# Kernel tuning notes

Measured on AMD Instinct MI355X. Metric: run time of the kernel, lower is better.

Reference implementation:

```python
import jax, jax.numpy as jnp
import numpy as np

N_NODES = 50000
N_EDGES = 800000
IN_CH = 128
OUT_CH = 64
HID = 2 * OUT_CH  # 128
NEG_SLOPE = 0.2  # PyG GATConv default negative_slope


def gat_conv(x, edge_index, W, a_src, a_dst, b):
    """Single-head PyG GATConv (heads=1, concat=True, self-loops already in edge_index)."""
    N = x.shape[0]
    h = x @ W  # [N, C]
    src, dst = edge_index[0], edge_index[1]
    # per-edge attention logits: leaky_relu(a_src . h_src + a_dst . h_dst)
    e = jax.nn.leaky_relu((h @ a_src)[src] + (h @ a_dst)[dst], NEG_SLOPE)  # [E]
    # softmax over incoming edges of each dst node (numerically stable)
    m = jax.ops.segment_max(e, dst, num_segments=N)
    p = jnp.exp(e - m[dst])
    denom = jax.ops.segment_sum(p, dst, num_segments=N)
    coef = p / denom[dst]  # [E]
    # scatter-aggregate weighted source features
    out = jax.ops.segment_sum(coef[:, None] * h[src], dst, num_segments=N)  # [N, C]
    return out + b


def setup_inputs() -> dict:
    key = jax.random.key(0)
    ks = jax.random.split(key, 12)
    s_in = 1.0 / np.sqrt(IN_CH)
    s_h = 1.0 / np.sqrt(HID)
    return {
        "x": jax.random.normal(ks[0], (N_NODES, IN_CH), dtype=jnp.float32),
        "edge_index": jax.random.randint(ks[1], (2, N_EDGES), 0, N_NODES, dtype=jnp.int64),
        "W1": jax.random.normal(ks[2], (IN_CH, HID), dtype=jnp.float32) * s_in,
        "a_src1": jax.random.normal(ks[3], (HID,), dtype=jnp.float32) * s_h,
        "a_dst1": jax.random.normal(ks[4], (HID,), dtype=jnp.float32) * s_h,
        "b1": jnp.zeros((HID,), dtype=jnp.float32),
        "W_mu": jax.random.normal(ks[5], (HID, OUT_CH), dtype=jnp.float32) * s_h,
        "a_src_mu": jax.random.normal(ks[6], (OUT_CH,), dtype=jnp.float32) * 0.125,
        "a_dst_mu": jax.random.normal(ks[7], (OUT_CH,), dtype=jnp.float32) * 0.125,
        "b_mu": jnp.zeros((OUT_CH,), dtype=jnp.float32),
        "W_ls": jax.random.normal(ks[8], (HID, OUT_CH), dtype=jnp.float32) * s_h,
        "a_src_ls": jax.random.normal(ks[9], (OUT_CH,), dtype=jnp.float32) * 0.125,
        "a_dst_ls": jax.random.normal(ks[10], (OUT_CH,), dtype=jnp.float32) * 0.125,
        "b_ls": jnp.zeros((OUT_CH,), dtype=jnp.float32),
    }


def reference(x, edge_index, W1, a_src1, a_dst1, b1, W_mu, a_src_mu, a_dst_mu, b_mu, W_ls, a_src_ls, a_dst_ls, b_ls):
    N = x.shape[0]
    loops = jnp.arange(N, dtype=edge_index.dtype)
    ei = jnp.concatenate([edge_index, jnp.stack([loops, loops])], axis=1)  # add self-loops
    h = jax.nn.relu(gat_conv(x, ei, W1, a_src1, a_dst1, b1))
    mu = gat_conv(h, ei, W_mu, a_src_mu, a_dst_mu, b_mu)
    logstd = gat_conv(h, ei, W_ls, a_src_ls, a_dst_ls, b_ls)
    return mu, logstd
```

## Files before the change

kernel.cpp:

```cpp
#include <hip/hip_runtime.h>
#include <hip/hip_bf16.h>
#include <math.h>

typedef __attribute__((ext_vector_type(8))) _Float16 half8;
typedef __attribute__((ext_vector_type(4))) float f32x4;


__device__ __forceinline__ float wave_max64(float v) {
#pragma unroll
  for (int o = 32; o > 0; o >>= 1) v = fmaxf(v, __shfl_xor(v, o));
  return v;
}
__device__ __forceinline__ float wave_sum64(float v) {
#pragma unroll
  for (int o = 32; o > 0; o >>= 1) v += __shfl_xor(v, o);
  return v;
}
__device__ __forceinline__ float leaky02(float v) { return v > 0.0f ? v : 0.2f * v; }

__device__ __forceinline__ unsigned short f2bf(float f) {
  unsigned u = __float_as_uint(f);
  u += 0x7FFF + ((u >> 16) & 1);
  return (unsigned short)(u >> 16);
}
__device__ __forceinline__ float2 bfp(unsigned v) {
  float2 r;
  r.x = __uint_as_float(v << 16);
  r.y = __uint_as_float(v & 0xFFFF0000u);
  return r;
}


#define BSHIFT 9
#define BDSTS 512

__global__ __launch_bounds__(256) void bucket_hist_kernel(
    const int* __restrict__ ei, int* __restrict__ bcount, int E, int NBUCK) {
  __shared__ int h[128];
  if (threadIdx.x < 128) h[threadIdx.x] = 0;
  __syncthreads();
  for (int e = blockIdx.x * blockDim.x + threadIdx.x; e < E; e += gridDim.x * blockDim.x)
    atomicAdd(&h[ei[E + e] >> BSHIFT], 1);
  __syncthreads();
  if (threadIdx.x < NBUCK && h[threadIdx.x]) atomicAdd(&bcount[threadIdx.x], h[threadIdx.x]);
}

__global__ __launch_bounds__(128) void bucket_scan_kernel(
    const int* __restrict__ bcount, int* __restrict__ bstart, int* __restrict__ bcursor,
    int* __restrict__ row_start, int NBUCK, int E, int N) {
  __shared__ int lds[128];
  int t = threadIdx.x;
  int v = (t < NBUCK) ? bcount[t] : 0;
  lds[t] = v;
  __syncthreads();
#pragma unroll
  for (int off = 1; off < 128; off <<= 1) {
    int tmp = (t >= off) ? lds[t - off] : 0;
    __syncthreads();
    lds[t] += tmp;
    __syncthreads();
  }
  if (t < NBUCK) {
    int excl = lds[t] - v;
    bstart[t] = excl;
    bcursor[t] = excl;
  }
  if (t == 0) { bstart[NBUCK] = E; row_start[N] = E; }
}

#define CHUNK 4096
__global__ __launch_bounds__(256) void pair_scatter_kernel(
    const int* __restrict__ ei, int* __restrict__ bcursor, int2* __restrict__ pairs, int E) {
  __shared__ int h[128], base[128], cur[128];
  if (threadIdx.x < 128) { h[threadIdx.x] = 0; cur[threadIdx.x] = 0; }
  __syncthreads();
  int c0 = blockIdx.x * CHUNK;
  int c1 = min(c0 + CHUNK, E);
  for (int e = c0 + (int)threadIdx.x; e < c1; e += 256)
    atomicAdd(&h[ei[E + e] >> BSHIFT], 1);
  __syncthreads();
  if (threadIdx.x < 128 && h[threadIdx.x])
    base[threadIdx.x] = atomicAdd(&bcursor[threadIdx.x], h[threadIdx.x]);
  __syncthreads();
  for (int e = c0 + (int)threadIdx.x; e < c1; e += 256) {
    int dst = ei[E + e];
    int src = ei[e];
    int b = dst >> BSHIFT;
    int r = atomicAdd(&cur[b], 1);
    pairs[base[b] + r] = make_int2(src, dst);
  }
}

__global__ __launch_bounds__(512) void fine_kernel(
    const int2* __restrict__ pairs, const int* __restrict__ bstart,
    int* __restrict__ row_start, int* __restrict__ esrc, int N) {
  __shared__ int h[BDSTS], sc[BDSTS], cur[BDSTS];
  int t = threadIdx.x;
  int b = blockIdx.x;
  int d0 = b << BSHIFT;
  int d1 = min(d0 + BDSTS, N);
  int beg = bstart[b], end = bstart[b + 1];
  h[t] = 0;
  __syncthreads();
  for (int i = beg + t; i < end; i += 512) atomicAdd(&h[pairs[i].y - d0], 1);
  __syncthreads();
  int v = h[t];
  sc[t] = v;
  __syncthreads();
#pragma unroll
  for (int off = 1; off < BDSTS; off <<= 1) {
    int tmp = (t >= off) ? sc[t - off] : 0;
    __syncthreads();
    sc[t] += tmp;
    __syncthreads();
  }
  int excl = sc[t] - v;
  if (d0 + t < d1) row_start[d0 + t] = beg + excl;
  cur[t] = excl;
  __syncthreads();
  for (int i = beg + t; i < end; i += 512) {
    int2 p = pairs[i];
    int r = atomicAdd(&cur[p.y - d0], 1);
    esrc[beg + r] = p.x;
  }
}


__global__ __launch_bounds__(256) void prep_w_kernel(
    const float* __restrict__ W1, const float* __restrict__ Wmu, const float* __restrict__ Wls,
    _Float16* __restrict__ Wt1, _Float16* __restrict__ Wt2) {
  int idx = blockIdx.x * 256 + threadIdx.x;
  int c = idx >> 7, k = idx & 127;
  Wt1[idx] = (_Float16)W1[k * 128 + c];
  float w2 = (c < 64) ? Wmu[k * 64 + c] : Wls[k * 64 + (c - 64)];
  Wt2[idx] = (_Float16)w2;
}


__global__ __launch_bounds__(256) void gemm1_mfma(
    const float* __restrict__ X, const _Float16* __restrict__ Wt,
    const float* __restrict__ a_src, const float* __restrict__ a_dst,
    unsigned short* __restrict__ Hb, float* __restrict__ asrc, float* __restrict__ adst, int N) {
  const int wid = threadIdx.x >> 6, lane = threadIdx.x & 63;
  const int r16 = (blockIdx.x * 4 + wid) * 16;
  if (r16 >= N) return;
  const int cg = lane & 15;
  const int kq = (lane >> 4) * 8;
  const int rA = r16 + cg;
  const int rowClamp = min(rA, N - 1);

  f32x4 acc[8];
#pragma unroll
  for (int j = 0; j < 8; ++j) acc[j] = (f32x4){0.f, 0.f, 0.f, 0.f};

#pragma unroll
  for (int ks = 0; ks < 4; ++ks) {
    const int k0 = ks * 32;
    const float* xp = X + (size_t)rowClamp * 128 + k0 + kq;
    float4 xa = *(const float4*)xp;
    float4 xb = *(const float4*)(xp + 4);
    half8 a;
    a[0] = (_Float16)xa.x; a[1] = (_Float16)xa.y; a[2] = (_Float16)xa.z; a[3] = (_Float16)xa.w;
    a[4] = (_Float16)xb.x; a[5] = (_Float16)xb.y; a[6] = (_Float16)xb.z; a[7] = (_Float16)xb.w;
#pragma unroll
    for (int j = 0; j < 8; ++j) {
      half8 b = *(const half8*)(Wt + (size_t)(16 * j + cg) * 128 + k0 + kq);
      acc[j] = __builtin_amdgcn_mfma_f32_16x16x32_f16(a, b, acc[j], 0, 0, 0);
    }
  }

  float as_[8], ds_[8];
#pragma unroll
  for (int j = 0; j < 8; ++j) { as_[j] = a_src[16 * j + cg]; ds_[j] = a_dst[16 * j + cg]; }
  const int rg = (lane >> 4) * 4;
#pragma unroll
  for (int reg = 0; reg < 4; ++reg) {
    int row = r16 + rg + reg;
    bool ok = row < N;
    float ps = 0.f, pd = 0.f;
#pragma unroll
    for (int j = 0; j < 8; ++j) {
      float v = acc[j][reg];
      if (ok) Hb[(size_t)row * 128 + 16 * j + cg] = f2bf(v);
      ps = fmaf(v, as_[j], ps);
      pd = fmaf(v, ds_[j], pd);
    }
#pragma unroll
    for (int o = 1; o < 16; o <<= 1) { ps += __shfl_xor(ps, o); pd += __shfl_xor(pd, o); }
    if (ok && cg == 0) { asrc[row] = ps; adst[row] = pd; }
  }
}

__global__ __launch_bounds__(256) void gemm2_mfma(
    const _Float16* __restrict__ Xh, const _Float16* __restrict__ Wt,
    const float* __restrict__ a_src_mu, const float* __restrict__ a_dst_mu,
    const float* __restrict__ a_src_ls, const float* __restrict__ a_dst_ls,
    unsigned short* __restrict__ Hb, float* __restrict__ as2, float* __restrict__ ad2, int N) {
  const int wid = threadIdx.x >> 6, lane = threadIdx.x & 63;
  const int r16 = (blockIdx.x * 4 + wid) * 16;
  if (r16 >= N) return;
  const int cg = lane & 15;
  const int kq = (lane >> 4) * 8;
  const int rA = r16 + cg;
  const int rowClamp = min(rA, N - 1);

  f32x4 acc[8];
#pragma unroll
  for (int j = 0; j < 8; ++j) acc[j] = (f32x4){0.f, 0.f, 0.f, 0.f};

#pragma unroll
  for (int ks = 0; ks < 4; ++ks) {
    const int k0 = ks * 32;
    half8 a = *(const half8*)(Xh + (size_t)rowClamp * 128 + k0 + kq);
#pragma unroll
    for (int j = 0; j < 8; ++j) {
      half8 b = *(const half8*)(Wt + (size_t)(16 * j + cg) * 128 + k0 + kq);
      acc[j] = __builtin_amdgcn_mfma_f32_16x16x32_f16(a, b, acc[j], 0, 0, 0);
    }
  }

  float asv[8], adv[8];
#pragma unroll
  for (int j = 0; j < 4; ++j) {
    asv[j] = a_src_mu[16 * j + cg]; adv[j] = a_dst_mu[16 * j + cg];
    asv[j + 4] = a_src_ls[16 * j + cg]; adv[j + 4] = a_dst_ls[16 * j + cg];
  }
  const int rg = (lane >> 4) * 4;
#pragma unroll
  for (int reg = 0; reg < 4; ++reg) {
    int row = r16 + rg + reg;
    bool ok = row < N;
    float psm = 0.f, pdm = 0.f, psl = 0.f, pdl = 0.f;
#pragma unroll
    for (int j = 0; j < 8; ++j) {
      float v = acc[j][reg];
      if (ok) Hb[(size_t)row * 128 + 16 * j + cg] = f2bf(v);
      if (j < 4) { psm = fmaf(v, asv[j], psm); pdm = fmaf(v, adv[j], pdm); }
      else       { psl = fmaf(v, asv[j], psl); pdl = fmaf(v, adv[j], pdl); }
    }
#pragma unroll
    for (int o = 1; o < 16; o <<= 1) {
      psm += __shfl_xor(psm, o); pdm += __shfl_xor(pdm, o);
      psl += __shfl_xor(psl, o); pdl += __shfl_xor(pdl, o);
    }
    if (ok && cg == 0) {
      as2[2 * row] = psm; ad2[2 * row] = pdm;
      as2[2 * row + 1] = psl; ad2[2 * row + 1] = pdl;
    }
  }
}


__global__ __launch_bounds__(256) void agg1_kernel(
    const unsigned short* __restrict__ Hb, const float* __restrict__ asrc,
    const float* __restrict__ adst,
    const int* __restrict__ row_start, const int* __restrict__ esrc,
    const float* __restrict__ b, _Float16* __restrict__ hout, int N) {
  int lane = threadIdx.x & 63;
  int d = (int)((blockIdx.x * blockDim.x + threadIdx.x) >> 6);
  if (d >= N) return;
  float ad = adst[d];
  float m = leaky02(asrc[d] + ad);
  float denom = 1.0f;
  float2 acc = bfp(((const unsigned*)(Hb + (size_t)d * 128))[lane]);
  int beg = row_start[d], end = row_start[d + 1];
  for (int base = beg; base < end; base += 64) {
    int nv = end - base;
    if (nv > 64) nv = 64;
    float e = -INFINITY;
    int s = 0;
    if (lane < nv) {
      s = esrc[base + lane];
      e = leaky02(asrc[s] + ad);
    }
    float cm = wave_max64(e);
    if (cm > m) {
      float sc = __expf(m - cm);
      denom *= sc; acc.x *= sc; acc.y *= sc;
      m = cm;
    }
    float w = __expf(e - m);
    denom += wave_sum64(w);
    int j = 0;
    for (; j + 4 <= nv; j += 4) {
      int s0 = __shfl(s, j), s1 = __shfl(s, j + 1), s2 = __shfl(s, j + 2), s3 = __shfl(s, j + 3);
      float w0 = __shfl(w, j), w1 = __shfl(w, j + 1), w2 = __shfl(w, j + 2), w3 = __shfl(w, j + 3);
      unsigned v0 = ((const unsigned*)(Hb + (size_t)s0 * 128))[lane];
      unsigned v1 = ((const unsigned*)(Hb + (size_t)s1 * 128))[lane];
      unsigned v2 = ((const unsigned*)(Hb + (size_t)s2 * 128))[lane];
      unsigned v3 = ((const unsigned*)(Hb + (size_t)s3 * 128))[lane];
      float2 f0 = bfp(v0), f1 = bfp(v1), f2 = bfp(v2), f3 = bfp(v3);
      acc.x = fmaf(w0, f0.x, acc.x); acc.y = fmaf(w0, f0.y, acc.y);
      acc.x = fmaf(w1, f1.x, acc.x); acc.y = fmaf(w1, f1.y, acc.y);
      acc.x = fmaf(w2, f2.x, acc.x); acc.y = fmaf(w2, f2.y, acc.y);
      acc.x = fmaf(w3, f3.x, acc.x); acc.y = fmaf(w3, f3.y, acc.y);
    }
    for (; j < nv; ++j) {
      int sj = __shfl(s, j);
      float wj = __shfl(w, j);
      float2 f = bfp(((const unsigned*)(Hb + (size_t)sj * 128))[lane]);
      acc.x = fmaf(wj, f.x, acc.x);
      acc.y = fmaf(wj, f.y, acc.y);
    }
  }
  float inv = 1.0f / denom;
  float2 bv = ((const float2*)b)[lane];
  float ox = fmaxf(fmaf(acc.x, inv, bv.x), 0.0f);
  float oy = fmaxf(fmaf(acc.y, inv, bv.y), 0.0f);
  _Float16 h2[2] = {(_Float16)ox, (_Float16)oy};
  ((unsigned*)(hout + (size_t)d * 128))[lane] = *(unsigned*)h2;
}


__global__ __launch_bounds__(256) void agg2_kernel(
    const unsigned short* __restrict__ Hb,
    const float2* __restrict__ as2, const float2* __restrict__ ad2,
    const int* __restrict__ row_start, const int* __restrict__ esrc,
    const float* __restrict__ b_mu, const float* __restrict__ b_ls,
    float* __restrict__ out_mu, float* __restrict__ out_ls, int N) {
  int lane = threadIdx.x & 63;
  int d = (int)((blockIdx.x * blockDim.x + threadIdx.x) >> 6);
  if (d >= N) return;
  bool isMu = lane < 32;
  float2 a2d = ad2[d];
  float2 a2s_self = as2[d];
  float m_mu = leaky02(a2s_self.x + a2d.x);
  float m_ls = leaky02(a2s_self.y + a2d.y);
  float den_mu = 1.0f, den_ls = 1.0f;
  float2 acc = bfp(((const unsigned*)(Hb + (size_t)d * 128))[lane]);
  int beg = row_start[d], end = row_start[d + 1];
  for (int base = beg; base < end; base += 64) {
    int nv = end - base;
    if (nv > 64) nv = 64;
    float e_mu = -INFINITY, e_ls = -INFINITY;
    int s = 0;
    if (lane < nv) {
      s = esrc[base + lane];
      float2 av = as2[s];
      e_mu = leaky02(av.x + a2d.x);
      e_ls = leaky02(av.y + a2d.y);
    }
    float cm_mu = wave_max64(e_mu);
    float cm_ls = wave_max64(e_ls);
    float sc_mu = 1.0f, sc_ls = 1.0f;
    if (cm_mu > m_mu) { sc_mu = __expf(m_mu - cm_mu); den_mu *= sc_mu; m_mu = cm_mu; }
    if (cm_ls > m_ls) { sc_ls = __expf(m_ls - cm_ls); den_ls *= sc_ls; m_ls = cm_ls; }
    float sc = isMu ? sc_mu : sc_ls;
    acc.x *= sc; acc.y *= sc;
    float w_mu = __expf(e_mu - m_mu);
    float w_ls = __expf(e_ls - m_ls);
    den_mu += wave_sum64(w_mu);
    den_ls += wave_sum64(w_ls);
    int j = 0;
    for (; j + 4 <= nv; j += 4) {
      int s0 = __shfl(s, j), s1 = __shfl(s, j + 1), s2 = __shfl(s, j + 2), s3 = __shfl(s, j + 3);
      float wm0 = __shfl(w_mu, j), wm1 = __shfl(w_mu, j + 1), wm2 = __shfl(w_mu, j + 2), wm3 = __shfl(w_mu, j + 3);
      float wl0 = __shfl(w_ls, j), wl1 = __shfl(w_ls, j + 1), wl2 = __shfl(w_ls, j + 2), wl3 = __shfl(w_ls, j + 3);
      float w0 = isMu ? wm0 : wl0, w1 = isMu ? wm1 : wl1, w2 = isMu ? wm2 : wl2, w3 = isMu ? wm3 : wl3;
      unsigned v0 = ((const unsigned*)(Hb + (size_t)s0 * 128))[lane];
      unsigned v1 = ((const unsigned*)(Hb + (size_t)s1 * 128))[lane];
      unsigned v2 = ((const unsigned*)(Hb + (size_t)s2 * 128))[lane];
      unsigned v3 = ((const unsigned*)(Hb + (size_t)s3 * 128))[lane];
      float2 f0 = bfp(v0), f1 = bfp(v1), f2 = bfp(v2), f3 = bfp(v3);
      acc.x = fmaf(w0, f0.x, acc.x); acc.y = fmaf(w0, f0.y, acc.y);
      acc.x = fmaf(w1, f1.x, acc.x); acc.y = fmaf(w1, f1.y, acc.y);
      acc.x = fmaf(w2, f2.x, acc.x); acc.y = fmaf(w2, f2.y, acc.y);
      acc.x = fmaf(w3, f3.x, acc.x); acc.y = fmaf(w3, f3.y, acc.y);
    }
    for (; j < nv; ++j) {
      float wj_mu = __shfl(w_mu, j);
      float wj_ls = __shfl(w_ls, j);
      float wj = isMu ? wj_mu : wj_ls;
      int sj = __shfl(s, j);
      float2 f = bfp(((const unsigned*)(Hb + (size_t)sj * 128))[lane]);
      acc.x = fmaf(wj, f.x, acc.x);
      acc.y = fmaf(wj, f.y, acc.y);
    }
  }
  float inv = isMu ? (1.0f / den_mu) : (1.0f / den_ls);
  float2 bv = isMu ? ((const float2*)b_mu)[lane] : ((const float2*)b_ls)[lane - 32];
  float2 o;
  o.x = fmaf(acc.x, inv, bv.x);
  o.y = fmaf(acc.y, inv, bv.y);
  if (isMu) ((float2*)(out_mu + (size_t)d * 64))[lane] = o;
  else      ((float2*)(out_ls + (size_t)d * 64))[lane - 32] = o;
}


extern "C" void kernel_launch(void* const* d_in, const int* in_sizes, int n_in,
                              void* d_out, int out_size, void* d_ws, size_t ws_size,
                              hipStream_t stream) {
  const float* x = (const float*)d_in[0];
  const int* ei = (const int*)d_in[1];
  const float* W1 = (const float*)d_in[2];
  const float* a_src1 = (const float*)d_in[3];
  const float* a_dst1 = (const float*)d_in[4];
  const float* b1 = (const float*)d_in[5];
  const float* W_mu = (const float*)d_in[6];
  const float* a_src_mu = (const float*)d_in[7];
  const float* a_dst_mu = (const float*)d_in[8];
  const float* b_mu = (const float*)d_in[9];
  const float* W_ls = (const float*)d_in[10];
  const float* a_src_ls = (const float*)d_in[11];
  const float* a_dst_ls = (const float*)d_in[12];
  const float* b_ls = (const float*)d_in[13];

  const int N = in_sizes[0] / 128;
  const int E = in_sizes[1] / 2;
  const int NBUCK = (N + BDSTS - 1) >> BSHIFT;

  uint8_t* p = (uint8_t*)d_ws;
  auto carve = [&](size_t bytes) -> void* {
    void* q = (void*)p;
    p += (bytes + 255) & ~(size_t)255;
    return q;
  };
  int* bcount = (int*)carve((size_t)(NBUCK + 1) * 4);
  int* bstart = (int*)carve((size_t)(NBUCK + 1) * 4);
  int* bcursor = (int*)carve((size_t)NBUCK * 4);
  int* row_start = (int*)carve((size_t)(N + 1) * 4);
  int* esrc = (int*)carve((size_t)E * 4);
  int2* pairs = (int2*)carve((size_t)E * 8);
  unsigned short* Hb1 = (unsigned short*)carve((size_t)N * 128 * 2);
  _Float16* h1 = (_Float16*)carve((size_t)N * 128 * 2);
  _Float16* Wt1 = (_Float16*)carve((size_t)128 * 128 * 2);
  _Float16* Wt2 = (_Float16*)carve((size_t)128 * 128 * 2);
  float* as1 = (float*)carve((size_t)N * 4);
  float* ad1 = (float*)carve((size_t)N * 4);
  float* as2 = (float*)carve((size_t)N * 8);
  float* ad2 = (float*)carve((size_t)N * 8);

  unsigned short* Hb2 = Hb1;

  hipMemsetAsync(bcount, 0, (size_t)(NBUCK + 1) * 4, stream);
  prep_w_kernel<<<64, 256, 0, stream>>>(W1, W_mu, W_ls, Wt1, Wt2);
  bucket_hist_kernel<<<(E + 2047) / 2048, 256, 0, stream>>>(ei, bcount, E, NBUCK);
  bucket_scan_kernel<<<1, 128, 0, stream>>>(bcount, bstart, bcursor, row_start, NBUCK, E, N);
  pair_scatter_kernel<<<(E + CHUNK - 1) / CHUNK, 256, 0, stream>>>(ei, bcursor, pairs, E);
  fine_kernel<<<NBUCK, 512, 0, stream>>>(pairs, bstart, row_start, esrc, N);

  gemm1_mfma<<<(N + 63) / 64, 256, 0, stream>>>(x, Wt1, a_src1, a_dst1, Hb1, as1, ad1, N);
  agg1_kernel<<<(N + 3) / 4, 256, 0, stream>>>(Hb1, as1, ad1, row_start, esrc, b1, h1, N);
  gemm2_mfma<<<(N + 63) / 64, 256, 0, stream>>>(h1, Wt2, a_src_mu, a_dst_mu,
                                                a_src_ls, a_dst_ls, Hb2, as2, ad2, N);
  float* out_mu = (float*)d_out;
  float* out_ls = out_mu + (size_t)N * 64;
  agg2_kernel<<<(N + 3) / 4, 256, 0, stream>>>(Hb2, (const float2*)as2, (const float2*)ad2,
                                               row_start, esrc, b_mu, b_ls, out_mu, out_ls, N);
}
```

Baseline: 183.9 us.

## Process two destination nodes per wavefront and pack sort pairs into 32 bits

The aggregation kernels now split each 64-lane wavefront into two 32-lane halves. Each half handles one destination node, and each lane loads 8 bytes (4 bf16 features) per neighbour instead of 4 bytes. With an average in-degree of about 17, this should cut the idle lanes in the 64-wide edge chunks and halve the per-node reduction and shuffle overhead. Separately, the CSR-build pairs are packed as (src<<9 | dst&511) in one 32-bit word, which halves the pair buffer traffic. The cost is that both halves loop until the larger degree of the two nodes, so degree imbalance wastes some work, and the packing assumes src fits in 23 bits.

New measurement: 165.6 us. 10.0% less time.

```diff
diff --git a/kernel.cpp b/kernel.cpp
--- a/kernel.cpp
+++ b/kernel.cpp
@@ -6,16 +6,6 @@
 typedef __attribute__((ext_vector_type(4))) float f32x4;
 
 
-__device__ __forceinline__ float wave_max64(float v) {
-#pragma unroll
-  for (int o = 32; o > 0; o >>= 1) v = fmaxf(v, __shfl_xor(v, o));
-  return v;
-}
-__device__ __forceinline__ float wave_sum64(float v) {
-#pragma unroll
-  for (int o = 32; o > 0; o >>= 1) v += __shfl_xor(v, o);
-  return v;
-}
 __device__ __forceinline__ float leaky02(float v) { return v > 0.0f ? v : 0.2f * v; }
 
 __device__ __forceinline__ unsigned short f2bf(float f) {
@@ -70,7 +60,7 @@
 
 #define CHUNK 4096
 __global__ __launch_bounds__(256) void pair_scatter_kernel(
-    const int* __restrict__ ei, int* __restrict__ bcursor, int2* __restrict__ pairs, int E) {
+    const int* __restrict__ ei, int* __restrict__ bcursor, unsigned* __restrict__ pairs, int E) {
   __shared__ int h[128], base[128], cur[128];
   if (threadIdx.x < 128) { h[threadIdx.x] = 0; cur[threadIdx.x] = 0; }
   __syncthreads();
@@ -87,12 +77,12 @@
     int src = ei[e];
     int b = dst >> BSHIFT;
     int r = atomicAdd(&cur[b], 1);
-    pairs[base[b] + r] = make_int2(src, dst);
+    pairs[base[b] + r] = ((unsigned)src << BSHIFT) | (unsigned)(dst & (BDSTS - 1));
   }
 }
 
 __global__ __launch_bounds__(512) void fine_kernel(
-    const int2* __restrict__ pairs, const int* __restrict__ bstart,
+    const unsigned* __restrict__ pairs, const int* __restrict__ bstart,
     int* __restrict__ row_start, int* __restrict__ esrc, int N) {
   __shared__ int h[BDSTS], sc[BDSTS], cur[BDSTS];
   int t = threadIdx.x;
@@ -102,7 +92,7 @@
   int beg = bstart[b], end = bstart[b + 1];
   h[t] = 0;
   __syncthreads();
-  for (int i = beg + t; i < end; i += 512) atomicAdd(&h[pairs[i].y - d0], 1);
+  for (int i = beg + t; i < end; i += 512) atomicAdd(&h[pairs[i] & (BDSTS - 1)], 1);
   __syncthreads();
   int v = h[t];
   sc[t] = v;
@@ -119,9 +109,9 @@
   cur[t] = excl;
   __syncthreads();
   for (int i = beg + t; i < end; i += 512) {
-    int2 p = pairs[i];
-    int r = atomicAdd(&cur[p.y - d0], 1);
-    esrc[beg + r] = p.x;
+    unsigned p = pairs[i];
+    int r = atomicAdd(&cur[p & (BDSTS - 1)], 1);
+    esrc[beg + r] = (int)(p >> BSHIFT);
   }
 }
 
@@ -251,139 +241,194 @@
 }
 
 
-__global__ __launch_bounds__(256) void agg1_kernel(
+__global__ __launch_bounds__(256) void agg1_pv(
     const unsigned short* __restrict__ Hb, const float* __restrict__ asrc,
-    const float* __restrict__ adst,
-    const int* __restrict__ row_start, const int* __restrict__ esrc,
-    const float* __restrict__ b, _Float16* __restrict__ hout, int N) {
-  int lane = threadIdx.x & 63;
-  int d = (int)((blockIdx.x * blockDim.x + threadIdx.x) >> 6);
-  if (d >= N) return;
-  float ad = adst[d];
-  float m = leaky02(asrc[d] + ad);
-  float denom = 1.0f;
-  float2 acc = bfp(((const unsigned*)(Hb + (size_t)d * 128))[lane]);
-  int beg = row_start[d], end = row_start[d + 1];
-  for (int base = beg; base < end; base += 64) {
-    int nv = end - base;
-    if (nv > 64) nv = 64;
-    float e = -INFINITY;
-    int s = 0;
-    if (lane < nv) {
-      s = esrc[base + lane];
-      e = leaky02(asrc[s] + ad);
-    }
-    float cm = wave_max64(e);
-    if (cm > m) {
-      float sc = __expf(m - cm);
-      denom *= sc; acc.x *= sc; acc.y *= sc;
-      m = cm;
-    }
+    const float* __restrict__ adst, const int* __restrict__ row_start,
+    const int* __restrict__ esrc, const float* __restrict__ b,
+    _Float16* __restrict__ hout, int N) {
+  const int lane = threadIdx.x & 63;
+  const int half = lane >> 5, sub = lane & 31;
+  const int g = (int)(blockIdx.x * 4 + (threadIdx.x >> 6));
+  const int d = g * 2 + half;
+  const bool dok = d < N;
+  const int dc = dok ? d : N - 1;
+  const float ad = adst[dc];
+  float m = leaky02(asrc[dc] + ad);
+  float den = 1.0f;
+  uint2 sv = *(const uint2*)(Hb + (size_t)dc * 128 + sub * 4);
+  float2 f0 = bfp(sv.x), f1 = bfp(sv.y);
+  float a0 = f0.x, a1 = f0.y, a2 = f1.x, a3 = f1.y;
+  const int beg = row_start[dc];
+  const int n = dok ? (row_start[dc + 1] - beg) : 0;
+  int nmax = n;
+#pragma unroll
+  for (int o = 32; o > 0; o >>= 1) nmax = max(nmax, __shfl_xor(nmax, o));
+  const int hbase = half * 32;
+  for (int c0 = 0; c0 < nmax; c0 += 32) {
+    int j = c0 + sub;
+    bool v = j < n;
+    int s = v ? esrc[beg + j] : dc;
+    float e = v ? leaky02(asrc[s] + ad) : -INFINITY;
+    float cm = e;
+#pragma unroll
+    for (int o = 16; o > 0; o >>= 1) cm = fmaxf(cm, __shfl_xor(cm, o));
+    float mn = fmaxf(m, cm);
+    float sc = __expf(m - mn);
+    m = mn;
+    den *= sc; a0 *= sc; a1 *= sc; a2 *= sc; a3 *= sc;
     float w = __expf(e - m);
-    denom += wave_sum64(w);
-    int j = 0;
-    for (; j + 4 <= nv; j += 4) {
-      int s0 = __shfl(s, j), s1 = __shfl(s, j + 1), s2 = __shfl(s, j + 2), s3 = __shfl(s, j + 3);
-      float w0 = __shfl(w, j), w1 = __shfl(w, j + 1), w2 = __shfl(w, j + 2), w3 = __shfl(w, j + 3);
-      unsigned v0 = ((const unsigned*)(Hb + (size_t)s0 * 128))[lane];
-      unsigned v1 = ((const unsigned*)(Hb + (size_t)s1 * 128))[lane];
-      unsigned v2 = ((const unsigned*)(Hb + (size_t)s2 * 128))[lane];
-      unsigned v3 = ((const unsigned*)(Hb + (size_t)s3 * 128))[lane];
-      float2 f0 = bfp(v0), f1 = bfp(v1), f2 = bfp(v2), f3 = bfp(v3);
-      acc.x = fmaf(w0, f0.x, acc.x); acc.y = fmaf(w0, f0.y, acc.y);
-      acc.x = fmaf(w1, f1.x, acc.x); acc.y = fmaf(w1, f1.y, acc.y);
-      acc.x = fmaf(w2, f2.x, acc.x); acc.y = fmaf(w2, f2.y, acc.y);
-      acc.x = fmaf(w3, f3.x, acc.x); acc.y = fmaf(w3, f3.y, acc.y);
-    }
-    for (; j < nv; ++j) {
-      int sj = __shfl(s, j);
-      float wj = __shfl(w, j);
-      float2 f = bfp(((const unsigned*)(Hb + (size_t)sj * 128))[lane]);
-      acc.x = fmaf(wj, f.x, acc.x);
-      acc.y = fmaf(wj, f.y, acc.y);
-    }
-  }
-  float inv = 1.0f / denom;
-  float2 bv = ((const float2*)b)[lane];
-  float ox = fmaxf(fmaf(acc.x, inv, bv.x), 0.0f);
-  float oy = fmaxf(fmaf(acc.y, inv, bv.y), 0.0f);
-  _Float16 h2[2] = {(_Float16)ox, (_Float16)oy};
-  ((unsigned*)(hout + (size_t)d * 128))[lane] = *(unsigned*)h2;
-}
-
-
-__global__ __launch_bounds__(256) void agg2_kernel(
+    float ws = w;
+#pragma unroll
+    for (int o = 16; o > 0; o >>= 1) ws += __shfl_xor(ws, o);
+    den += ws;
+    int cnt = n - c0; if (cnt > 32) cnt = 32;
+    int jj = 0;
+    for (; jj + 4 <= cnt; jj += 4) {
+      int s0 = __shfl(s, hbase + jj), s1 = __shfl(s, hbase + jj + 1);
+      int s2 = __shfl(s, hbase + jj + 2), s3 = __shfl(s, hbase + jj + 3);
+      float w0 = __shfl(w, hbase + jj), w1 = __shfl(w, hbase + jj + 1);
+      float w2 = __shfl(w, hbase + jj + 2), w3 = __shfl(w, hbase + jj + 3);
+      uint2 h0 = *(const uint2*)(Hb + (size_t)s0 * 128 + sub * 4);
+      uint2 h1 = *(const uint2*)(Hb + (size_t)s1 * 128 + sub * 4);
+      uint2 h2 = *(const uint2*)(Hb + (size_t)s2 * 128 + sub * 4);
+      uint2 h3 = *(const uint2*)(Hb + (size_t)s3 * 128 + sub * 4);
+      float2 p0 = bfp(h0.x), p1 = bfp(h0.y);
+      a0 = fmaf(w0, p0.x, a0); a1 = fmaf(w0, p0.y, a1); a2 = fmaf(w0, p1.x, a2); a3 = fmaf(w0, p1.y, a3);
+      p0 = bfp(h1.x); p1 = bfp(h1.y);
+      a0 = fmaf(w1, p0.x, a0); a1 = fmaf(w1, p0.y, a1); a2 = fmaf(w1, p1.x, a2); a3 = fmaf(w1, p1.y, a3);
+      p0 = bfp(h2.x); p1 = bfp(h2.y);
+      a0 = fmaf(w2, p0.x, a0); a1 = fmaf(w2, p0.y, a1); a2 = fmaf(w2, p1.x, a2); a3 = fmaf(w2, p1.y, a3);
+      p0 = bfp(h3.x); p1 = bfp(h3.y);
+      a0 = fmaf(w3, p0.x, a0); a1 = fmaf(w3, p0.y, a1); a2 = fmaf(w3, p1.x, a2); a3 = fmaf(w3, p1.y, a3);
+    }
+    for (; jj < cnt; ++jj) {
+      int sj = __shfl(s, hbase + jj);
+      float wj = __shfl(w, hbase + jj);
+      uint2 hv = *(const uint2*)(Hb + (size_t)sj * 128 + sub * 4);
+      float2 p0 = bfp(hv.x), p1 = bfp(hv.y);
+      a0 = fmaf(wj, p0.x, a0); a1 = fmaf(wj, p0.y, a1);
+      a2 = fmaf(wj, p1.x, a2); a3 = fmaf(wj, p1.y, a3);
+    }
+  }
+  if (dok) {
+    float inv = 1.0f / den;
+    float4 bv = *(const float4*)(b + sub * 4);
+    _Float16 o4[4];
+    o4[0] = (_Float16)fmaxf(fmaf(a0, inv, bv.x), 0.f);
+    o4[1] = (_Float16)fmaxf(fmaf(a1, inv, bv.y), 0.f);
+    o4[2] = (_Float16)fmaxf(fmaf(a2, inv, bv.z), 0.f);
+    o4[3] = (_Float16)fmaxf(fmaf(a3, inv, bv.w), 0.f);
+    *(uint2*)(hout + (size_t)d * 128 + sub * 4) = *(uint2*)o4;
+  }
+}
+
+
+__global__ __launch_bounds__(256) void agg2_pv(
     const unsigned short* __restrict__ Hb,
     const float2* __restrict__ as2, const float2* __restrict__ ad2,
     const int* __restrict__ row_start, const int* __restrict__ esrc,
     const float* __restrict__ b_mu, const float* __restrict__ b_ls,
     float* __restrict__ out_mu, float* __restrict__ out_ls, int N) {
-  int lane = threadIdx.x & 63;
-  int d = (int)((blockIdx.x * blockDim.x + threadIdx.x) >> 6);
-  if (d >= N) return;
-  bool isMu = lane < 32;
-  float2 a2d = ad2[d];
-  float2 a2s_self = as2[d];
-  float m_mu = leaky02(a2s_self.x + a2d.x);
-  float m_ls = leaky02(a2s_self.y + a2d.y);
-  float den_mu = 1.0f, den_ls = 1.0f;
-  float2 acc = bfp(((const unsigned*)(Hb + (size_t)d * 128))[lane]);
-  int beg = row_start[d], end = row_start[d + 1];
-  for (int base = beg; base < end; base += 64) {
-    int nv = end - base;
-    if (nv > 64) nv = 64;
-    float e_mu = -INFINITY, e_ls = -INFINITY;
-    int s = 0;
-    if (lane < nv) {
-      s = esrc[base + lane];
+  const int lane = threadIdx.x & 63;
+  const int half = lane >> 5, sub = lane & 31;
+  const bool isMu = sub < 16;
+  const int g = (int)(blockIdx.x * 4 + (threadIdx.x >> 6));
+  const int d = g * 2 + half;
+  const bool dok = d < N;
+  const int dc = dok ? d : N - 1;
+  const float2 adv = ad2[dc];
+  const float2 asv = as2[dc];
+  float mm = leaky02(asv.x + adv.x);
+  float ml = leaky02(asv.y + adv.y);
+  float den_m = 1.0f, den_l = 1.0f;
+  uint2 sv = *(const uint2*)(Hb + (size_t)dc * 128 + sub * 4);
+  float2 f0 = bfp(sv.x), f1 = bfp(sv.y);
+  float a0 = f0.x, a1 = f0.y, a2 = f1.x, a3 = f1.y;
+  const int beg = row_start[dc];
+  const int n = dok ? (row_start[dc + 1] - beg) : 0;
+  int nmax = n;
+#pragma unroll
+  for (int o = 32; o > 0; o >>= 1) nmax = max(nmax, __shfl_xor(nmax, o));
+  const int hbase = half * 32;
+  for (int c0 = 0; c0 < nmax; c0 += 32) {
+    int j = c0 + sub;
+    bool v = j < n;
+    int s = v ? esrc[beg + j] : dc;
+    float em = -INFINITY, el = -INFINITY;
+    if (v) {
       float2 av = as2[s];
-      e_mu = leaky02(av.x + a2d.x);
-      e_ls = leaky02(av.y + a2d.y);
-    }
-    float cm_mu = wave_max64(e_mu);
-    float cm_ls = wave_max64(e_ls);
-    float sc_mu = 1.0f, sc_ls = 1.0f;
-    if (cm_mu > m_mu) { sc_mu = __expf(m_mu - cm_mu); den_mu *= sc_mu; m_mu = cm_mu; }
-    if (cm_ls > m_ls) { sc_ls = __expf(m_ls - cm_ls); den_ls *= sc_ls; m_ls = cm_ls; }
-    float sc = isMu ? sc_mu : sc_ls;
-    acc.x *= sc; acc.y *= sc;
-    float w_mu = __expf(e_mu - m_mu);
-    float w_ls = __expf(e_ls - m_ls);
-    den_mu += wave_sum64(w_mu);
-    den_ls += wave_sum64(w_ls);
-    int j = 0;
-    for (; j + 4 <= nv; j += 4) {
-      int s0 = __shfl(s, j), s1 = __shfl(s, j + 1), s2 = __shfl(s, j + 2), s3 = __shfl(s, j + 3);
-      float wm0 = __shfl(w_mu, j), wm1 = __shfl(w_mu, j + 1), wm2 = __shfl(w_mu, j + 2), wm3 = __shfl(w_mu, j + 3);
-      float wl0 = __shfl(w_ls, j), wl1 = __shfl(w_ls, j + 1), wl2 = __shfl(w_ls, j + 2), wl3 = __shfl(w_ls, j + 3);
-      float w0 = isMu ? wm0 : wl0, w1 = isMu ? wm1 : wl1, w2 = isMu ? wm2 : wl2, w3 = isMu ? wm3 : wl3;
-      unsigned v0 = ((const unsigned*)(Hb + (size_t)s0 * 128))[lane];
-      unsigned v1 = ((const unsigned*)(Hb + (size_t)s1 * 128))[lane];
-      unsigned v2 = ((const unsigned*)(Hb + (size_t)s2 * 128))[lane];
-      unsigned v3 = ((const unsigned*)(Hb + (size_t)s3 * 128))[lane];
-      float2 f0 = bfp(v0), f1 = bfp(v1), f2 = bfp(v2), f3 = bfp(v3);
-      acc.x = fmaf(w0, f0.x, acc.x); acc.y = fmaf(w0, f0.y, acc.y);
-      acc.x = fmaf(w1, f1.x, acc.x); acc.y = fmaf(w1, f1.y, acc.y);
-      acc.x = fmaf(w2, f2.x, acc.x); acc.y = fmaf(w2, f2.y, acc.y);
-      acc.x = fmaf(w3, f3.x, acc.x); acc.y = fmaf(w3, f3.y, acc.y);
-    }
-    for (; j < nv; ++j) {
-      float wj_mu = __shfl(w_mu, j);
-      float wj_ls = __shfl(w_ls, j);
-      float wj = isMu ? wj_mu : wj_ls;
-      int sj = __shfl(s, j);
-      float2 f = bfp(((const unsigned*)(Hb + (size_t)sj * 128))[lane]);
-      acc.x = fmaf(wj, f.x, acc.x);
-      acc.y = fmaf(wj, f.y, acc.y);
-    }
-  }
-  float inv = isMu ? (1.0f / den_mu) : (1.0f / den_ls);
-  float2 bv = isMu ? ((const float2*)b_mu)[lane] : ((const float2*)b_ls)[lane - 32];
-  float2 o;
-  o.x = fmaf(acc.x, inv, bv.x);
-  o.y = fmaf(acc.y, inv, bv.y);
-  if (isMu) ((float2*)(out_mu + (size_t)d * 64))[lane] = o;
-  else      ((float2*)(out_ls + (size_t)d * 64))[lane - 32] = o;
+      em = leaky02(av.x + adv.x);
+      el = leaky02(av.y + adv.y);
+    }
+    float cmm = em, cml = el;
+#pragma unroll
+    for (int o = 16; o > 0; o >>= 1) {
+      cmm = fmaxf(cmm, __shfl_xor(cmm, o));
+      cml = fmaxf(cml, __shfl_xor(cml, o));
+    }
+    float mnm = fmaxf(mm, cmm), mnl = fmaxf(ml, cml);
+    float scm = __expf(mm - mnm), scl = __expf(ml - mnl);
+    mm = mnm; ml = mnl;
+    den_m *= scm; den_l *= scl;
+    float sce = isMu ? scm : scl;
+    a0 *= sce; a1 *= sce; a2 *= sce; a3 *= sce;
+    float wm = __expf(em - mm), wl = __expf(el - ml);
+    float wsm = wm, wsl = wl;
+#pragma unroll
+    for (int o = 16; o > 0; o >>= 1) {
+      wsm += __shfl_xor(wsm, o);
+      wsl += __shfl_xor(wsl, o);
+    }
+    den_m += wsm; den_l += wsl;
+    int cnt = n - c0; if (cnt > 32) cnt = 32;
+    int jj = 0;
+    for (; jj + 4 <= cnt; jj += 4) {
+      int s0 = __shfl(s, hbase + jj), s1 = __shfl(s, hbase + jj + 1);
+      int s2 = __shfl(s, hbase + jj + 2), s3 = __shfl(s, hbase + jj + 3);
+      float wm0 = __shfl(wm, hbase + jj), wm1 = __shfl(wm, hbase + jj + 1);
+      float wm2 = __shfl(wm, hbase + jj + 2), wm3 = __shfl(wm, hbase + jj + 3);
+      float wl0 = __shfl(wl, hbase + jj), wl1 = __shfl(wl, hbase + jj + 1);
+      float wl2 = __shfl(wl, hbase + jj + 2), wl3 = __shfl(wl, hbase + jj + 3);
+      float w0 = isMu ? wm0 : wl0, w1 = isMu ? wm1 : wl1;
+      float w2 = isMu ? wm2 : wl2, w3 = isMu ? wm3 : wl3;
+      uint2 h0 = *(const uint2*)(Hb + (size_t)s0 * 128 + sub * 4);
+      uint2 h1 = *(const uint2*)(Hb + (size_t)s1 * 128 + sub * 4);
+      uint2 h2 = *(const uint2*)(Hb + (size_t)s2 * 128 + sub * 4);
+      uint2 h3 = *(const uint2*)(Hb + (size_t)s3 * 128 + sub * 4);
+      float2 p0 = bfp(h0.x), p1 = bfp(h0.y);
+      a0 = fmaf(w0, p0.x, a0); a1 = fmaf(w0, p0.y, a1); a2 = fmaf(w0, p1.x, a2); a3 = fmaf(w0, p1.y, a3);
+      p0 = bfp(h1.x); p1 = bfp(h1.y);
+      a0 = fmaf(w1, p0.x, a0); a1 = fmaf(w1, p0.y, a1); a2 = fmaf(w1, p1.x, a2); a3 = fmaf(w1, p1.y, a3);
+      p0 = bfp(h2.x); p1 = bfp(h2.y);
+      a0 = fmaf(w2, p0.x, a0); a1 = fmaf(w2, p0.y, a1); a2 = fmaf(w2, p1.x, a2); a3 = fmaf(w2, p1.y, a3);
+      p0 = bfp(h3.x); p1 = bfp(h3.y);
+      a0 = fmaf(w3, p0.x, a0); a1 = fmaf(w3, p0.y, a1); a2 = fmaf(w3, p1.x, a2); a3 = fmaf(w3, p1.y, a3);
+    }
+    for (; jj < cnt; ++jj) {
+      int sj = __shfl(s, hbase + jj);
+      float wmj = __shfl(wm, hbase + jj);
+      float wlj = __shfl(wl, hbase + jj);
+      float wj = isMu ? wmj : wlj;
+      uint2 hv = *(const uint2*)(Hb + (size_t)sj * 128 + sub * 4);
+      float2 p0 = bfp(hv.x), p1 = bfp(hv.y);
+      a0 = fmaf(wj, p0.x, a0); a1 = fmaf(wj, p0.y, a1);
+      a2 = fmaf(wj, p1.x, a2); a3 = fmaf(wj, p1.y, a3);
+    }
+  }
+  if (dok) {
+    float inv = isMu ? (1.0f / den_m) : (1.0f / den_l);
+    const float* bp;
+    float* op;
+    if (isMu) { bp = b_mu + sub * 4; op = out_mu + (size_t)d * 64 + sub * 4; }
+    else      { bp = b_ls + sub * 4 - 64; op = out_ls + (size_t)d * 64 + sub * 4 - 64; }
+    float4 bv = *(const float4*)bp;
+    float4 o;
+    o.x = fmaf(a0, inv, bv.x);
+    o.y = fmaf(a1, inv, bv.y);
+    o.z = fmaf(a2, inv, bv.z);
+    o.w = fmaf(a3, inv, bv.w);
+    *(float4*)op = o;
+  }
 }
 
 
@@ -420,7 +465,7 @@
   int* bcursor = (int*)carve((size_t)NBUCK * 4);
   int* row_start = (int*)carve((size_t)(N + 1) * 4);
   int* esrc = (int*)carve((size_t)E * 4);
-  int2* pairs = (int2*)carve((size_t)E * 8);
+  unsigned* pairs = (unsigned*)carve((size_t)E * 4);
   unsigned short* Hb1 = (unsigned short*)carve((size_t)N * 128 * 2);
   _Float16* h1 = (_Float16*)carve((size_t)N * 128 * 2);
   _Float16* Wt1 = (_Float16*)carve((size_t)128 * 128 * 2);
@@ -440,11 +485,13 @@
   fine_kernel<<<NBUCK, 512, 0, stream>>>(pairs, bstart, row_start, esrc, N);
 
   gemm1_mfma<<<(N + 63) / 64, 256, 0, stream>>>(x, Wt1, a_src1, a_dst1, Hb1, as1, ad1, N);
-  agg1_kernel<<<(N + 3) / 4, 256, 0, stream>>>(Hb1, as1, ad1, row_start, esrc, b1, h1, N);
+  const int nwaves = (N + 1) / 2;
+  const int nblk = (nwaves + 3) / 4;
+  agg1_pv<<<nblk, 256, 0, stream>>>(Hb1, as1, ad1, row_start, esrc, b1, h1, N);
   gemm2_mfma<<<(N + 63) / 64, 256, 0, stream>>>(h1, Wt2, a_src_mu, a_dst_mu,
                                                 a_src_ls, a_dst_ls, Hb2, as2, ad2, N);
   float* out_mu = (float*)d_out;
   float* out_ls = out_mu + (size_t)N * 64;
-  agg2_kernel<<<(N + 3) / 4, 256, 0, stream>>>(Hb2, (const float2*)as2, (const float2*)ad2,
-                                               row_start, esrc, b_mu, b_ls, out_mu, out_ls, N);
-}
+  agg2_pv<<<nblk, 256, 0, stream>>>(Hb2, (const float2*)as2, (const float2*)ad2,
+                                    row_start, esrc, b_mu, b_ls, out_mu, out_ls, N);
+}
```
